# Kernel optimization log

Hardware: AMD Instinct MI355X
Metric: run time of the kernel (lower is better)

## Reference

```python
import jax, jax.numpy as jnp
import numpy as np

N = 100000  # nodes
E = 600000  # edges
D = 128     # input_dim
H = D // 2  # hidden of MLP head
OUT = 10    # output_dim
EPS = 1e-5
NEG_SLOPE = 0.2


def _p(key, shape, scale):
    return jax.random.normal(key, shape, dtype=jnp.float32) * scale


def setup_inputs() -> dict:
    key = jax.random.key(0)
    ks = jax.random.split(key, 16)
    s = 1.0 / np.sqrt(D)
    return {
        "x": jax.random.normal(ks[0], (N, D), dtype=jnp.float32),
        "edge_index": jax.random.randint(ks[1], (2, E), 0, N, dtype=jnp.int64),
        # SAGEConv: lin_l (applied to mean-aggregated neighbors, has bias), lin_r (root)
        "sage_Wl": _p(ks[2], (D, D), s), "sage_Wr": _p(ks[3], (D, D), s),
        "sage_b": jnp.zeros((D,), jnp.float32),
        # GCNConv
        "gcn_W": _p(ks[4], (D, D), s), "gcn_b": jnp.zeros((D,), jnp.float32),
        # GATConv (heads=1)
        "gat_W": _p(ks[5], (D, D), s),
        "gat_att_src": _p(ks[6], (D,), s), "gat_att_dst": _p(ks[7], (D,), s),
        "gat_b": jnp.zeros((D,), jnp.float32),
        # BatchNorms (batch-stat normalization)
        "bn1_g": jnp.ones((D,), jnp.float32), "bn1_b": jnp.zeros((D,), jnp.float32),
        "bn2_g": jnp.ones((D,), jnp.float32), "bn2_b": jnp.zeros((D,), jnp.float32),
        "bn3_g": jnp.ones((D,), jnp.float32), "bn3_b": jnp.zeros((D,), jnp.float32),
        # MLP head
        "lin1_W": _p(ks[8], (D, H), s), "lin1_b": jnp.zeros((H,), jnp.float32),
        "lin2_W": _p(ks[9], (H, OUT), 1.0 / np.sqrt(H)), "lin2_b": jnp.zeros((OUT,), jnp.float32),
    }


def _bn_relu(x, g, b):
    mu = jnp.mean(x, axis=0)
    var = jnp.mean(jnp.square(x - mu), axis=0)
    return jax.nn.relu((x - mu) * jax.lax.rsqrt(var + EPS) * g + b)


def _sage(x, src, dst, Wl, Wr, b):
    agg = jax.ops.segment_sum(x[src], dst, num_segments=N)          # [N, D]
    cnt = jax.ops.segment_sum(jnp.ones((src.shape[0],), x.dtype), dst, num_segments=N)
    mean = agg / jnp.maximum(cnt, 1.0)[:, None]
    return mean @ Wl + x @ Wr + b


def _gcn(x, src, dst, W, b):
    loop = jnp.arange(N, dtype=src.dtype)
    s = jnp.concatenate([src, loop]); d = jnp.concatenate([dst, loop])
    deg = jax.ops.segment_sum(jnp.ones((d.shape[0],), x.dtype), d, num_segments=N)
    dinv = jnp.where(deg > 0, jax.lax.rsqrt(jnp.maximum(deg, 1.0)), 0.0)
    xw = x @ W
    msg = xw[s] * (dinv[s] * dinv[d])[:, None]
    return jax.ops.segment_sum(msg, d, num_segments=N) + b


def _gat(x, src, dst, W, att_s, att_d, b):
    loop = jnp.arange(N, dtype=src.dtype)
    s = jnp.concatenate([src, loop]); d = jnp.concatenate([dst, loop])
    xw = x @ W                                  # [N, D]
    a_s = xw @ att_s                            # [N]
    a_d = xw @ att_d                            # [N]
    e = jax.nn.leaky_relu(a_s[s] + a_d[d], NEG_SLOPE)  # [E+N]
    m = jax.ops.segment_max(e, d, num_segments=N)
    ee = jnp.exp(e - m[d])
    z = jax.ops.segment_sum(ee, d, num_segments=N)
    alpha = ee / z[d]
    return jax.ops.segment_sum(alpha[:, None] * xw[s], d, num_segments=N) + b


def reference(x, edge_index, sage_Wl, sage_Wr, sage_b, gcn_W, gcn_b,
              gat_W, gat_att_src, gat_att_dst, gat_b,
              bn1_g, bn1_b, bn2_g, bn2_b, bn3_g, bn3_b,
              lin1_W, lin1_b, lin2_W, lin2_b):
    src, dst = edge_index[0], edge_index[1]
    h = _bn_relu(_sage(x, src, dst, sage_Wl, sage_Wr, sage_b), bn1_g, bn1_b)
    h = _bn_relu(_gcn(h, src, dst, gcn_W, gcn_b), bn2_g, bn2_b)
    h = _bn_relu(_gat(h, src, dst, gat_W, gat_att_src, gat_att_dst, gat_b), bn3_g, bn3_b)
    # dropout is identity in eval mode
    h = jax.nn.relu(h @ lin1_W + lin1_b) @ lin2_W + lin2_b
    return jax.nn.log_softmax(h, axis=1)
```

## Files before the change

### kernel.cpp

```cpp
#include <hip/hip_runtime.h>

static constexpr int Dd = 128;
static constexpr int Hh = 64;
static constexpr int OC = 10;
#define CDIV(a,b) (((a)+(b)-1)/(b))

typedef __attribute__((ext_vector_type(8))) short short8v;
typedef __attribute__((ext_vector_type(16))) float f32x16;
typedef unsigned short u16;

__device__ __forceinline__ float lrelu(float x){ return x>0.f? x : 0.2f*x; }
__device__ __forceinline__ unsigned f2bf(float f){
  unsigned u = __float_as_uint(f);
  return (u + 0x7FFFu + ((u>>16)&1u)) >> 16;
}
__device__ __forceinline__ float bl(unsigned u){ return __uint_as_float(u<<16); }
__device__ __forceinline__ float bh(unsigned u){ return __uint_as_float(u & 0xFFFF0000u); }

__global__ __launch_bounds__(256) void k_hist(const int* __restrict__ dst, int E,
    int* __restrict__ cnt) {
  int e = blockIdx.x*256 + threadIdx.x;
  if (e < E) atomicAdd(cnt + dst[e], 1);
}

__global__ __launch_bounds__(256) void k_scan_l1(const int* __restrict__ cnt,
    int* __restrict__ rp, int n, int* __restrict__ bsum) {
  __shared__ int sdata[256];
  int t = threadIdx.x;
  int base = blockIdx.x*2048 + t*8;
  int v[8]; int s = 0;
  #pragma unroll
  for (int k = 0; k < 8; k++) { v[k] = (base+k < n) ? cnt[base+k] : 0; s += v[k]; }
  sdata[t] = s; __syncthreads();
  for (int off = 1; off < 256; off <<= 1) {
    int a = sdata[t];
    int b = (t >= off) ? sdata[t-off] : 0;
    __syncthreads();
    sdata[t] = a + b;
    __syncthreads();
  }
  int ex = sdata[t] - s;
  if (t == 255) bsum[blockIdx.x] = sdata[255];
  int run = ex;
  #pragma unroll
  for (int k = 0; k < 8; k++) { if (base+k < n) rp[base+k] = run; run += v[k]; }
}

__global__ void k_scan_l2(int* __restrict__ bsum, int nb) {
  if (threadIdx.x == 0 && blockIdx.x == 0) {
    int run = 0;
    for (int i = 0; i < nb; i++) { int v = bsum[i]; bsum[i] = run; run += v; }
  }
}

__global__ __launch_bounds__(256) void k_scan_l3(int* __restrict__ rp, int n,
    const int* __restrict__ bsum, int E) {
  int off = bsum[blockIdx.x];
  int base = blockIdx.x*2048 + threadIdx.x*8;
  #pragma unroll
  for (int k = 0; k < 8; k++) if (base+k < n) rp[base+k] += off;
  if (blockIdx.x == 0 && threadIdx.x == 0) rp[n] = E;
}

__global__ __launch_bounds__(256) void k_fill(const int* __restrict__ src,
    const int* __restrict__ dst, int E, const int* __restrict__ rp,
    int* __restrict__ cnt, int* __restrict__ col) {
  int e = blockIdx.x*256 + threadIdx.x;
  if (e >= E) return;
  int d = dst[e];
  int pos = rp[d] + atomicSub(cnt + d, 1) - 1;
  col[pos] = src[e];
}

__global__ __launch_bounds__(256) void k_dinv(const int* __restrict__ rp,
    float* __restrict__ dinv, int n) {
  int i = blockIdx.x*256 + threadIdx.x;
  if (i < n) dinv[i] = rsqrtf((float)(rp[i+1] - rp[i]) + 1.0f);
}

__global__ __launch_bounds__(256) void k_wt_all(
    const float* __restrict__ w0, const float* __restrict__ w1,
    const float* __restrict__ w2, const float* __restrict__ w3,
    const float* __restrict__ w4,
    u16* __restrict__ o0, u16* __restrict__ o1, u16* __restrict__ o2,
    u16* __restrict__ o3, u16* __restrict__ o4) {
  int idx = blockIdx.x*256 + threadIdx.x;
  const float* W; u16* O; int base, N;
  if (idx < 65536) {
    int m = idx >> 14;
    W = m==0?w0 : m==1?w1 : m==2?w2 : w3;
    O = m==0?o0 : m==1?o1 : m==2?o2 : o3;
    base = idx & 16383; N = 128;
  } else if (idx < 73728) {
    W = w4; O = o4; base = idx - 65536; N = 64;
  } else return;
  int n = base / 128, k = base % 128;
  int kc = k >> 3, nf = n >> 5, lm = n & 31;
  int fi = (((kc*(N>>5) + nf)*32 + lm) << 3) | (k & 7);
  O[fi] = (u16)f2bf(W[k*N + n]);
}

__global__ __launch_bounds__(256) void k_tobf16(const float* __restrict__ in,
    u16* __restrict__ out, int n8) {
  int idx = blockIdx.x*256 + threadIdx.x;
  if (idx >= n8) return;
  const float4* p = reinterpret_cast<const float4*>(in) + idx*2;
  float4 v0 = p[0], v1 = p[1];
  uint4 w;
  w.x = f2bf(v0.x) | (f2bf(v0.y)<<16);
  w.y = f2bf(v0.z) | (f2bf(v0.w)<<16);
  w.z = f2bf(v1.x) | (f2bf(v1.y)<<16);
  w.w = f2bf(v1.z) | (f2bf(v1.w)<<16);
  reinterpret_cast<uint4*>(out)[idx] = w;
}

__global__ __launch_bounds__(256) void k_sage_gather(const u16* __restrict__ xb,
    const int* __restrict__ rp, const int* __restrict__ col,
    u16* __restrict__ ob, int n) {
  int gid = blockIdx.x*256 + threadIdx.x;
  int i = gid >> 5, l = gid & 31;
  if (i >= n) return;
  int beg = rp[i], end = rp[i+1];
  const u16* xp = xb + l*4;
  float a0=0.f, a1=0.f, a2=0.f, a3=0.f;
  int j = beg;
  if (j + 4 <= end) {
    int s0=col[j], s1=col[j+1], s2=col[j+2], s3=col[j+3];
    uint2 c0 = *reinterpret_cast<const uint2*>(xp + (size_t)s0*Dd);
    uint2 c1 = *reinterpret_cast<const uint2*>(xp + (size_t)s1*Dd);
    uint2 c2 = *reinterpret_cast<const uint2*>(xp + (size_t)s2*Dd);
    uint2 c3 = *reinterpret_cast<const uint2*>(xp + (size_t)s3*Dd);
    j += 4;
    for (; j + 4 <= end; j += 4) {
      int t0=col[j], t1=col[j+1], t2=col[j+2], t3=col[j+3];
      uint2 n0 = *reinterpret_cast<const uint2*>(xp + (size_t)t0*Dd);
      uint2 n1 = *reinterpret_cast<const uint2*>(xp + (size_t)t1*Dd);
      uint2 n2 = *reinterpret_cast<const uint2*>(xp + (size_t)t2*Dd);
      uint2 n3 = *reinterpret_cast<const uint2*>(xp + (size_t)t3*Dd);
      a0 += (bl(c0.x)+bl(c1.x)) + (bl(c2.x)+bl(c3.x));
      a1 += (bh(c0.x)+bh(c1.x)) + (bh(c2.x)+bh(c3.x));
      a2 += (bl(c0.y)+bl(c1.y)) + (bl(c2.y)+bl(c3.y));
      a3 += (bh(c0.y)+bh(c1.y)) + (bh(c2.y)+bh(c3.y));
      c0=n0; c1=n1; c2=n2; c3=n3;
    }
    a0 += (bl(c0.x)+bl(c1.x)) + (bl(c2.x)+bl(c3.x));
    a1 += (bh(c0.x)+bh(c1.x)) + (bh(c2.x)+bh(c3.x));
    a2 += (bl(c0.y)+bl(c1.y)) + (bl(c2.y)+bl(c3.y));
    a3 += (bh(c0.y)+bh(c1.y)) + (bh(c2.y)+bh(c3.y));
  }
  for (; j < end; j++) {
    int s = col[j];
    uint2 v = *reinterpret_cast<const uint2*>(xp + (size_t)s*Dd);
    a0 += bl(v.x); a1 += bh(v.x); a2 += bl(v.y); a3 += bh(v.y);
  }
  float inv = 1.0f / fmaxf((float)(end - beg), 1.0f);
  uint2 o;
  o.x = f2bf(a0*inv) | (f2bf(a1*inv)<<16);
  o.y = f2bf(a2*inv) | (f2bf(a3*inv)<<16);
  *reinterpret_cast<uint2*>(ob + (size_t)i*Dd + l*4) = o;
}

__global__ __launch_bounds__(256) void k_gcn_gather(const u16* __restrict__ xb,
    const int* __restrict__ rp, const int* __restrict__ col,
    const float* __restrict__ dinv, u16* __restrict__ ob, int n) {
  int gid = blockIdx.x*256 + threadIdx.x;
  int i = gid >> 5, l = gid & 31;
  if (i >= n) return;
  int beg = rp[i], end = rp[i+1];
  const u16* xp = xb + l*4;
  float a0=0.f, a1=0.f, a2=0.f, a3=0.f;
  int j = beg;
  if (j + 4 <= end) {
    int s0=col[j], s1=col[j+1], s2=col[j+2], s3=col[j+3];
    uint2 c0 = *reinterpret_cast<const uint2*>(xp + (size_t)s0*Dd);
    uint2 c1 = *reinterpret_cast<const uint2*>(xp + (size_t)s1*Dd);
    uint2 c2 = *reinterpret_cast<const uint2*>(xp + (size_t)s2*Dd);
    uint2 c3 = *reinterpret_cast<const uint2*>(xp + (size_t)s3*Dd);
    float w0 = dinv[s0], w1 = dinv[s1], w2 = dinv[s2], w3 = dinv[s3];
    j += 4;
    for (; j + 4 <= end; j += 4) {
      int t0=col[j], t1=col[j+1], t2=col[j+2], t3=col[j+3];
      uint2 n0 = *reinterpret_cast<const uint2*>(xp + (size_t)t0*Dd);
      uint2 n1 = *reinterpret_cast<const uint2*>(xp + (size_t)t1*Dd);
      uint2 n2 = *reinterpret_cast<const uint2*>(xp + (size_t)t2*Dd);
      uint2 n3 = *reinterpret_cast<const uint2*>(xp + (size_t)t3*Dd);
      float x0 = dinv[t0], x1 = dinv[t1], x2 = dinv[t2], x3 = dinv[t3];
      a0 += (w0*bl(c0.x)+w1*bl(c1.x)) + (w2*bl(c2.x)+w3*bl(c3.x));
      a1 += (w0*bh(c0.x)+w1*bh(c1.x)) + (w2*bh(c2.x)+w3*bh(c3.x));
      a2 += (w0*bl(c0.y)+w1*bl(c1.y)) + (w2*bl(c2.y)+w3*bl(c3.y));
      a3 += (w0*bh(c0.y)+w1*bh(c1.y)) + (w2*bh(c2.y)+w3*bh(c3.y));
      c0=n0; c1=n1; c2=n2; c3=n3;
      w0=x0; w1=x1; w2=x2; w3=x3;
    }
    a0 += (w0*bl(c0.x)+w1*bl(c1.x)) + (w2*bl(c2.x)+w3*bl(c3.x));
    a1 += (w0*bh(c0.x)+w1*bh(c1.x)) + (w2*bh(c2.x)+w3*bh(c3.x));
    a2 += (w0*bl(c0.y)+w1*bl(c1.y)) + (w2*bl(c2.y)+w3*bl(c3.y));
    a3 += (w0*bh(c0.y)+w1*bh(c1.y)) + (w2*bh(c2.y)+w3*bh(c3.y));
  }
  for (; j < end; j++) {
    int s = col[j];
    float w = dinv[s];
    uint2 v = *reinterpret_cast<const uint2*>(xp + (size_t)s*Dd);
    a0 += w*bl(v.x); a1 += w*bh(v.x); a2 += w*bl(v.y); a3 += w*bh(v.y);
  }
  float di = dinv[i];
  float ws = di*di;
  uint2 sv = *reinterpret_cast<const uint2*>(xp + (size_t)i*Dd);
  a0 = di*a0 + ws*bl(sv.x); a1 = di*a1 + ws*bh(sv.x);
  a2 = di*a2 + ws*bl(sv.y); a3 = di*a3 + ws*bh(sv.y);
  uint2 o;
  o.x = f2bf(a0) | (f2bf(a1)<<16);
  o.y = f2bf(a2) | (f2bf(a3)<<16);
  *reinterpret_cast<uint2*>(ob + (size_t)i*Dd + l*4) = o;
}

__global__ __launch_bounds__(256) void k_gat_gather(const u16* __restrict__ xb,
    const int* __restrict__ rp, const int* __restrict__ col,
    const float* __restrict__ a_s, const float* __restrict__ a_d,
    u16* __restrict__ ob, int n) {
  int gid = blockIdx.x*256 + threadIdx.x;
  int i = gid >> 5, l = gid & 31;
  if (i >= n) return;
  int beg = rp[i], end = rp[i+1];
  const u16* xp = xb + l*4;
  float ad = a_d[i];
  float m = lrelu(a_s[i] + ad);
  float z = 1.0f;
  uint2 sv = *reinterpret_cast<const uint2*>(xp + (size_t)i*Dd);
  float a0 = bl(sv.x), a1 = bh(sv.x), a2 = bl(sv.y), a3 = bh(sv.y);
  int j = beg;
  if (j + 4 <= end) {
    int s0=col[j], s1=col[j+1], s2=col[j+2], s3=col[j+3];
    uint2 c0 = *reinterpret_cast<const uint2*>(xp + (size_t)s0*Dd);
    uint2 c1 = *reinterpret_cast<const uint2*>(xp + (size_t)s1*Dd);
    uint2 c2 = *reinterpret_cast<const uint2*>(xp + (size_t)s2*Dd);
    uint2 c3 = *reinterpret_cast<const uint2*>(xp + (size_t)s3*Dd);
    float f0 = a_s[s0], f1 = a_s[s1], f2 = a_s[s2], f3 = a_s[s3];
    j += 4;
    for (; j + 4 <= end; j += 4) {
      int t0=col[j], t1=col[j+1], t2=col[j+2], t3=col[j+3];
      uint2 n0 = *reinterpret_cast<const uint2*>(xp + (size_t)t0*Dd);
      uint2 n1 = *reinterpret_cast<const uint2*>(xp + (size_t)t1*Dd);
      uint2 n2 = *reinterpret_cast<const uint2*>(xp + (size_t)t2*Dd);
      uint2 n3 = *reinterpret_cast<const uint2*>(xp + (size_t)t3*Dd);
      float g0 = a_s[t0], g1 = a_s[t1], g2 = a_s[t2], g3 = a_s[t3];
      float e0 = lrelu(f0+ad), e1 = lrelu(f1+ad);
      float e2 = lrelu(f2+ad), e3 = lrelu(f3+ad);
      float mg = fmaxf(fmaxf(e0,e1), fmaxf(e2,e3));
      if (mg > m) {
        float r = __expf(m - mg);
        z *= r; a0 *= r; a1 *= r; a2 *= r; a3 *= r;
        m = mg;
      }
      float w0 = __expf(e0-m), w1 = __expf(e1-m);
      float w2 = __expf(e2-m), w3 = __expf(e3-m);
      z += (w0+w1) + (w2+w3);
      a0 += (w0*bl(c0.x)+w1*bl(c1.x)) + (w2*bl(c2.x)+w3*bl(c3.x));
      a1 += (w0*bh(c0.x)+w1*bh(c1.x)) + (w2*bh(c2.x)+w3*bh(c3.x));
      a2 += (w0*bl(c0.y)+w1*bl(c1.y)) + (w2*bl(c2.y)+w3*bl(c3.y));
      a3 += (w0*bh(c0.y)+w1*bh(c1.y)) + (w2*bh(c2.y)+w3*bh(c3.y));
      c0=n0; c1=n1; c2=n2; c3=n3;
      f0=g0; f1=g1; f2=g2; f3=g3;
    }
    float e0 = lrelu(f0+ad), e1 = lrelu(f1+ad);
    float e2 = lrelu(f2+ad), e3 = lrelu(f3+ad);
    float mg = fmaxf(fmaxf(e0,e1), fmaxf(e2,e3));
    if (mg > m) {
      float r = __expf(m - mg);
      z *= r; a0 *= r; a1 *= r; a2 *= r; a3 *= r;
      m = mg;
    }
    float w0 = __expf(e0-m), w1 = __expf(e1-m);
    float w2 = __expf(e2-m), w3 = __expf(e3-m);
    z += (w0+w1) + (w2+w3);
    a0 += (w0*bl(c0.x)+w1*bl(c1.x)) + (w2*bl(c2.x)+w3*bl(c3.x));
    a1 += (w0*bh(c0.x)+w1*bh(c1.x)) + (w2*bh(c2.x)+w3*bh(c3.x));
    a2 += (w0*bl(c0.y)+w1*bl(c1.y)) + (w2*bl(c2.y)+w3*bl(c3.y));
    a3 += (w0*bh(c0.y)+w1*bh(c1.y)) + (w2*bh(c2.y)+w3*bh(c3.y));
  }
  for (; j < end; j++) {
    int s = col[j];
    uint2 v = *reinterpret_cast<const uint2*>(xp + (size_t)s*Dd);
    float e = lrelu(a_s[s]+ad);
    if (e > m) {
      float r = __expf(m - e);
      z *= r; a0 *= r; a1 *= r; a2 *= r; a3 *= r;
      m = e;
    }
    float w = __expf(e-m);
    z += w;
    a0 += w*bl(v.x); a1 += w*bh(v.x); a2 += w*bl(v.y); a3 += w*bh(v.y);
  }
  float inv = 1.0f / z;
  uint2 o;
  o.x = f2bf(a0*inv) | (f2bf(a1*inv)<<16);
  o.y = f2bf(a2*inv) | (f2bf(a3*inv)<<16);
  *reinterpret_cast<uint2*>(ob + (size_t)i*Dd + l*4) = o;
}

__global__ __launch_bounds__(256) void k_bn_stats_bf(const u16* __restrict__ X, int M,
    float* __restrict__ gsum, float* __restrict__ gsq) {
  __shared__ float ss[2][256];
  int t = threadIdx.x;
  int cd = t & 63;
  int rg = t >> 6;
  float s0=0.f, q0=0.f, s1=0.f, q1=0.f;
  const unsigned* Xu = reinterpret_cast<const unsigned*>(X);
  for (int r = blockIdx.x*4 + rg; r < M; r += gridDim.x*4) {
    unsigned v = Xu[(size_t)r*64 + cd];
    float a = bl(v), b = bh(v);
    s0 += a; q0 += a*a; s1 += b; q1 += b*b;
  }
  ss[0][t] = s0; ss[1][t] = q0; __syncthreads();
  float rs0 = 0.f, rq0 = 0.f;
  if (rg == 0) {
    rs0 = ss[0][cd] + ss[0][cd+64] + ss[0][cd+128] + ss[0][cd+192];
    rq0 = ss[1][cd] + ss[1][cd+64] + ss[1][cd+128] + ss[1][cd+192];
  }
  __syncthreads();
  ss[0][t] = s1; ss[1][t] = q1; __syncthreads();
  if (rg == 0) {
    float rs1 = ss[0][cd] + ss[0][cd+64] + ss[0][cd+128] + ss[0][cd+192];
    float rq1 = ss[1][cd] + ss[1][cd+64] + ss[1][cd+128] + ss[1][cd+192];
    atomicAdd(gsum + 2*cd,     rs0); atomicAdd(gsq + 2*cd,     rq0);
    atomicAdd(gsum + 2*cd + 1, rs1); atomicAdd(gsq + 2*cd + 1, rq1);
  }
}

template<int NCOLS, bool DUAL, bool BNA, bool STATS, bool BIASRELU, bool ATT, bool OUTBF, bool HEAD>
__global__ __launch_bounds__(256) void k_mm(
    const u16* __restrict__ A1, const u16* __restrict__ A2,
    const u16* __restrict__ WT1, const u16* __restrict__ WT2,
    const float* __restrict__ bng, const float* __restrict__ bnb,
    const float* __restrict__ bsum_in, const float* __restrict__ bsq_in,
    const float* __restrict__ bias,
    void* __restrict__ Cout, int M,
    float* __restrict__ gsum, float* __restrict__ gsq,
    const float* __restrict__ att_sv, const float* __restrict__ att_dv,
    float* __restrict__ as_out, float* __restrict__ ad_out,
    const float* __restrict__ W2, const float* __restrict__ b2) {
  constexpr int NF = NCOLS/32;
  __shared__ char ldsA[128*272];
  __shared__ char ldsW[NCOLS*256];
  __shared__ float s_scale[128], s_shift[128];
  __shared__ float s_sum[128], s_sq[128];
  __shared__ float w2s[Hh][OC];
  __shared__ float b2s[OC];
  int t = threadIdx.x;
  int wave = t >> 6, l = t & 63;
  int lm = l & 31, h = l >> 5;
  int row0 = blockIdx.x*128;

  if constexpr (BNA) {
    if (t < 128) {
      float mu = bsum_in[t] / (float)M;
      float var = fmaxf(bsq_in[t] / (float)M - mu*mu, 0.f);
      float sc = bng[t] * rsqrtf(var + 1e-5f);
      s_scale[t] = sc;
      s_shift[t] = bnb[t] - mu*sc;
    }
  }
  if constexpr (STATS) {
    if (t < 128) { s_sum[t] = 0.f; s_sq[t] = 0.f; }
  }
  if constexpr (HEAD) {
    for (int i = t; i < Hh*OC; i += 256) w2s[i/OC][i%OC] = W2[i];
    if (t < OC) b2s[t] = b2[t];
  }
  if (BNA || STATS || HEAD) __syncthreads();

  f32x16 acc[NF];
  #pragma unroll
  for (int nf = 0; nf < NF; nf++)
    #pragma unroll
    for (int i = 0; i < 16; i++) acc[nf][i] = 0.f;

  const int nph = DUAL ? 2 : 1;
  for (int ph = 0; ph < nph; ph++) {
    if (ph) __syncthreads();
    const u16* A = (DUAL && ph) ? A2 : A1;
    const u16* WT = (DUAL && ph) ? WT2 : WT1;
    #pragma unroll
    for (int i = 0; i < 8; i++) {
      int c = i*256 + t; int row = c >> 4; int k0 = (c & 15) << 3;
      uint4 w = {0,0,0,0};
      if (row0 + row < M)
        w = *reinterpret_cast<const uint4*>(A + (size_t)(row0+row)*128 + k0);
      if constexpr (BNA) {
        float4 sc0 = *reinterpret_cast<const float4*>(&s_scale[k0]);
        float4 sc1 = *reinterpret_cast<const float4*>(&s_scale[k0+4]);
        float4 sh0 = *reinterpret_cast<const float4*>(&s_shift[k0]);
        float4 sh1 = *reinterpret_cast<const float4*>(&s_shift[k0+4]);
        float e0 = fmaxf(bl(w.x)*sc0.x+sh0.x, 0.f), e1 = fmaxf(bh(w.x)*sc0.y+sh0.y, 0.f);
        float e2 = fmaxf(bl(w.y)*sc0.z+sh0.z, 0.f), e3 = fmaxf(bh(w.y)*sc0.w+sh0.w, 0.f);
        float e4 = fmaxf(bl(w.z)*sc1.x+sh1.x, 0.f), e5 = fmaxf(bh(w.z)*sc1.y+sh1.y, 0.f);
        float e6 = fmaxf(bl(w.w)*sc1.z+sh1.z, 0.f), e7 = fmaxf(bh(w.w)*sc1.w+sh1.w, 0.f);
        w.x = f2bf(e0) | (f2bf(e1)<<16);
        w.y = f2bf(e2) | (f2bf(e3)<<16);
        w.z = f2bf(e4) | (f2bf(e5)<<16);
        w.w = f2bf(e6) | (f2bf(e7)<<16);
      }
      *reinterpret_cast<uint4*>(ldsA + row*272 + k0*2) = w;
    }
    #pragma unroll
    for (int i = 0; i < NCOLS/16; i++) {
      int c = i*256 + t;
      reinterpret_cast<uint4*>(ldsW)[c] = reinterpret_cast<const uint4*>(WT)[c];
    }
    __syncthreads();
    #pragma unroll
    for (int ks = 0; ks < 8; ks++) {
      int kc = ks*2 + h;
      int arow = wave*32 + lm;
      short8v af = *reinterpret_cast<short8v*>(ldsA + arow*272 + kc*16);
      #pragma unroll
      for (int nf = 0; nf < NF; nf++) {
        short8v bf = *reinterpret_cast<short8v*>(ldsW + ((kc*NF + nf)*32 + lm)*16);
        acc[nf] = __builtin_amdgcn_mfma_f32_32x32x16_bf16(af, bf, acc[nf], 0, 0, 0);
      }
    }
  }
  if constexpr (HEAD) {
    __syncthreads();
    float* mrow = reinterpret_cast<float*>(ldsA);
    #pragma unroll
    for (int nf = 0; nf < NF; nf++) {
      int colg = nf*32 + lm;
      float bv = bias[colg];
      #pragma unroll
      for (int reg = 0; reg < 16; reg++) {
        int row = wave*32 + (reg&3) + 8*(reg>>2) + 4*h;
        mrow[row*65 + colg] = fmaxf(acc[nf][reg] + bv, 0.f);
      }
    }
    __syncthreads();
    if (t < 128) {
      int row = row0 + t;
      if (row < M) {
        float p[OC];
        #pragma unroll
        for (int c = 0; c < OC; c++) p[c] = b2s[c];
        for (int k = 0; k < Hh; k++) {
          float a = mrow[t*65 + k];
          #pragma unroll
          for (int c = 0; c < OC; c++) p[c] += a * w2s[k][c];
        }
        float mx = p[0];
        #pragma unroll
        for (int c = 1; c < OC; c++) mx = fmaxf(mx, p[c]);
        float s = 0.f;
        #pragma unroll
        for (int c = 0; c < OC; c++) s += __expf(p[c] - mx);
        float lse = mx + __logf(s);
        #pragma unroll
        for (int c = 0; c < OC; c++)
          ((float*)Cout)[(size_t)row*OC + c] = p[c] - lse;
      }
    }
    return;
  }
  #pragma unroll
  for (int nf = 0; nf < NF; nf++) {
    int colg = nf*32 + lm;
    float bv = 0.f;
    if constexpr (BIASRELU) bv = bias[colg];
    float ps = 0.f, pq = 0.f;
    #pragma unroll
    for (int reg = 0; reg < 16; reg++) {
      int row = row0 + wave*32 + (reg&3) + 8*(reg>>2) + 4*h;
      float v = acc[nf][reg];
      if constexpr (BIASRELU) v = fmaxf(v + bv, 0.f);
      if (row < M) {
        if constexpr (OUTBF)
          ((u16*)Cout)[(size_t)row*NCOLS + colg] = (u16)f2bf(v);
        else
          ((float*)Cout)[(size_t)row*NCOLS + colg] = v;
      }
      ps += v; pq += v*v;
    }
    if constexpr (STATS) {
      atomicAdd(&s_sum[colg], ps);
      atomicAdd(&s_sq[colg], pq);
    }
  }
  if constexpr (ATT) {
    float as_c[NF], ad_c[NF];
    #pragma unroll
    for (int nf = 0; nf < NF; nf++) { as_c[nf] = att_sv[nf*32+lm]; ad_c[nf] = att_dv[nf*32+lm]; }
    #pragma unroll
    for (int reg = 0; reg < 16; reg++) {
      float ps = 0.f, pd = 0.f;
      #pragma unroll
      for (int nf = 0; nf < NF; nf++) { float v = acc[nf][reg]; ps += v*as_c[nf]; pd += v*ad_c[nf]; }
      #pragma unroll
      for (int mm = 1; mm < 32; mm <<= 1) { ps += __shfl_xor(ps, mm); pd += __shfl_xor(pd, mm); }
      int row = row0 + wave*32 + (reg&3) + 8*(reg>>2) + 4*h;
      if (lm == 0 && row < M) { as_out[row] = ps; ad_out[row] = pd; }
    }
  }
  if constexpr (STATS) {
    __syncthreads();
    if (t < 128) { atomicAdd(gsum + t, s_sum[t]); atomicAdd(gsq + t, s_sq[t]); }
  }
}

extern "C" void kernel_launch(void* const* d_in, const int* in_sizes, int n_in,
                              void* d_out, int out_size, void* d_ws, size_t ws_size,
                              hipStream_t stream) {
  const float* x       = (const float*)d_in[0];
  const int*   ei      = (const int*)d_in[1];
  const float* sage_Wl = (const float*)d_in[2];
  const float* sage_Wr = (const float*)d_in[3];
  const float* gcn_W   = (const float*)d_in[5];
  const float* gat_W   = (const float*)d_in[7];
  const float* att_s   = (const float*)d_in[8];
  const float* att_d   = (const float*)d_in[9];
  const float* bn1_g = (const float*)d_in[11], *bn1_b = (const float*)d_in[12];
  const float* bn2_g = (const float*)d_in[13], *bn2_b = (const float*)d_in[14];
  const float* bn3_g = (const float*)d_in[15], *bn3_b = (const float*)d_in[16];
  const float* lin1_W = (const float*)d_in[17], *lin1_b = (const float*)d_in[18];
  const float* lin2_W = (const float*)d_in[19], *lin2_b = (const float*)d_in[20];

  const int Nn = in_sizes[0] / Dd;
  const int Ee = in_sizes[1] / 2;
  const int* srcv = ei;
  const int* dstv = ei + Ee;

  u16* b0 = (u16*)d_ws;
  u16* b1 = b0 + (size_t)Nn*Dd;
  u16* b2 = b1 + (size_t)Nn*Dd;
  float* dinv  = (float*)(b2 + (size_t)Nn*Dd);
  float* a_s   = dinv + Nn;
  float* a_d   = a_s + Nn;
  float* bs    = a_d + Nn;
  float* bs1_sum = bs,        *bs1_sq = bs + 128;
  float* bs2_sum = bs + 256,  *bs2_sq = bs + 384;
  float* bs3_sum = bs + 512,  *bs3_sq = bs + 640;
  int* rp    = (int*)(bs + 768);
  int* cnt_i = rp + (Nn + 1);
  int* bsum  = cnt_i + Nn;
  int* col   = bsum + 64;
  u16* wt_sWl = (u16*)(col + Ee);
  u16* wt_sWr = wt_sWl + 128*128;
  u16* wt_gcn = wt_sWr + 128*128;
  u16* wt_gat = wt_gcn + 128*128;
  u16* wt_l1  = wt_gat + 128*128;

  const dim3 B(256);
  const dim3 Gn(CDIV(Nn, 256));
  const dim3 Gn32(CDIV(Nn*32, 256));
  const dim3 Ge(CDIV(Ee, 256));
  const dim3 Gmm(CDIV(Nn, 128));
  const dim3 Gstat(512);
  const int nscan = CDIV(Nn, 2048);

  hipMemsetAsync(cnt_i, 0, (size_t)Nn*sizeof(int), stream);
  hipMemsetAsync(bs, 0, 768*sizeof(float), stream);

  k_hist<<<Ge, B, 0, stream>>>(dstv, Ee, cnt_i);
  k_scan_l1<<<dim3(nscan), B, 0, stream>>>(cnt_i, rp, Nn, bsum);
  k_scan_l2<<<dim3(1), dim3(64), 0, stream>>>(bsum, nscan);
  k_scan_l3<<<dim3(nscan), B, 0, stream>>>(rp, Nn, bsum, Ee);
  k_fill<<<Ge, B, 0, stream>>>(srcv, dstv, Ee, rp, cnt_i, col);
  k_dinv<<<Gn, B, 0, stream>>>(rp, dinv, Nn);
  k_wt_all<<<dim3(288), B, 0, stream>>>(sage_Wl, sage_Wr, gcn_W, gat_W, lin1_W,
                                        wt_sWl, wt_sWr, wt_gcn, wt_gat, wt_l1);
  k_tobf16<<<dim3(CDIV(Nn*Dd/8, 256)), B, 0, stream>>>(x, b0, Nn*Dd/8);

  k_sage_gather<<<Gn32, B, 0, stream>>>(b0, rp, col, b1, Nn);
  k_mm<128, true, false, true, false, false, true, false><<<Gmm, B, 0, stream>>>(
      b1, b0, wt_sWl, wt_sWr, nullptr, nullptr, nullptr, nullptr, nullptr,
      b2, Nn, bs1_sum, bs1_sq, nullptr, nullptr, nullptr, nullptr, nullptr, nullptr);

  k_mm<128, false, true, false, false, false, true, false><<<Gmm, B, 0, stream>>>(
      b2, nullptr, wt_gcn, nullptr, bn1_g, bn1_b, bs1_sum, bs1_sq, nullptr,
      b0, Nn, nullptr, nullptr, nullptr, nullptr, nullptr, nullptr, nullptr, nullptr);
  k_gcn_gather<<<Gn32, B, 0, stream>>>(b0, rp, col, dinv, b1, Nn);
  k_bn_stats_bf<<<Gstat, B, 0, stream>>>(b1, Nn, bs2_sum, bs2_sq);

  k_mm<128, false, true, false, false, true, true, false><<<Gmm, B, 0, stream>>>(
      b1, nullptr, wt_gat, nullptr, bn2_g, bn2_b, bs2_sum, bs2_sq, nullptr,
      b2, Nn, nullptr, nullptr, att_s, att_d, a_s, a_d, nullptr, nullptr);
  k_gat_gather<<<Gn32, B, 0, stream>>>(b2, rp, col, a_s, a_d, b0, Nn);
  k_bn_stats_bf<<<Gstat, B, 0, stream>>>(b0, Nn, bs3_sum, bs3_sq);

  k_mm<64, false, true, false, true, false, false, true><<<Gmm, B, 0, stream>>>(
      b0, nullptr, wt_l1, nullptr, bn3_g, bn3_b, bs3_sum, bs3_sq, lin1_b,
      (float*)d_out, Nn, nullptr, nullptr, nullptr, nullptr, nullptr, nullptr,
      lin2_W, lin2_b);
}
```

Measured before the change: 379.8 us.

## Stream GEMM weights through LDS in halves and merge shared scratch arrays

Weights are re-laid out nf-major so each GEMM block can load half the output columns' weights into LDS at a time, halving the ldsW footprint. The separate BN scale/shift, stats and head-weight shared arrays are merged into one aux buffer to cut LDS further. The aim is higher occupancy (more blocks per CU) in the fused GEMM kernels. The cost is an extra barrier and a second weight load per phase.

```diff
diff --git a/kernel.cpp b/kernel.cpp
--- a/kernel.cpp
+++ b/kernel.cpp
@@ -96,7 +96,7 @@
   } else return;
   int n = base / 128, k = base % 128;
   int kc = k >> 3, nf = n >> 5, lm = n & 31;
-  int fi = (((kc*(N>>5) + nf)*32 + lm) << 3) | (k & 7);
+  int fi = (((nf*16 + kc)*32 + lm) << 3) | (k & 7);
   O[fi] = (u16)f2bf(W[k*N + n]);
 }
 
@@ -339,13 +339,11 @@
     const float* __restrict__ att_sv, const float* __restrict__ att_dv,
     float* __restrict__ as_out, float* __restrict__ ad_out,
     const float* __restrict__ W2, const float* __restrict__ b2) {
-  constexpr int NF = NCOLS/32;
+  constexpr int NF  = NCOLS/32;
+  constexpr int NFH = NF/2;
   __shared__ char ldsA[128*272];
-  __shared__ char ldsW[NCOLS*256];
-  __shared__ float s_scale[128], s_shift[128];
-  __shared__ float s_sum[128], s_sq[128];
-  __shared__ float w2s[Hh][OC];
-  __shared__ float b2s[OC];
+  __shared__ char ldsW[NFH*16*32*16];
+  __shared__ float s_aux[640];
   int t = threadIdx.x;
   int wave = t >> 6, l = t & 63;
   int lm = l & 31, h = l >> 5;
@@ -356,18 +354,14 @@
       float mu = bsum_in[t] / (float)M;
       float var = fmaxf(bsq_in[t] / (float)M - mu*mu, 0.f);
       float sc = bng[t] * rsqrtf(var + 1e-5f);
-      s_scale[t] = sc;
-      s_shift[t] = bnb[t] - mu*sc;
+      s_aux[t] = sc;
+      s_aux[128 + t] = bnb[t] - mu*sc;
     }
   }
   if constexpr (STATS) {
-    if (t < 128) { s_sum[t] = 0.f; s_sq[t] = 0.f; }
-  }
-  if constexpr (HEAD) {
-    for (int i = t; i < Hh*OC; i += 256) w2s[i/OC][i%OC] = W2[i];
-    if (t < OC) b2s[t] = b2[t];
-  }
-  if (BNA || STATS || HEAD) __syncthreads();
+    if (t < 128) { s_aux[256 + t] = 0.f; s_aux[384 + t] = 0.f; }
+  }
+  if (BNA || STATS) __syncthreads();
 
   f32x16 acc[NF];
   #pragma unroll
@@ -387,10 +381,10 @@
       if (row0 + row < M)
         w = *reinterpret_cast<const uint4*>(A + (size_t)(row0+row)*128 + k0);
       if constexpr (BNA) {
-        float4 sc0 = *reinterpret_cast<const float4*>(&s_scale[k0]);
-        float4 sc1 = *reinterpret_cast<const float4*>(&s_scale[k0+4]);
-        float4 sh0 = *reinterpret_cast<const float4*>(&s_shift[k0]);
-        float4 sh1 = *reinterpret_cast<const float4*>(&s_shift[k0+4]);
+        float4 sc0 = *reinterpret_cast<const float4*>(&s_aux[k0]);
+        float4 sc1 = *reinterpret_cast<const float4*>(&s_aux[k0+4]);
+        float4 sh0 = *reinterpret_cast<const float4*>(&s_aux[128+k0]);
+        float4 sh1 = *reinterpret_cast<const float4*>(&s_aux[128+k0+4]);
         float e0 = fmaxf(bl(w.x)*sc0.x+sh0.x, 0.f), e1 = fmaxf(bh(w.x)*sc0.y+sh0.y, 0.f);
         float e2 = fmaxf(bl(w.y)*sc0.z+sh0.z, 0.f), e3 = fmaxf(bh(w.y)*sc0.w+sh0.w, 0.f);
         float e4 = fmaxf(bl(w.z)*sc1.x+sh1.x, 0.f), e5 = fmaxf(bh(w.z)*sc1.y+sh1.y, 0.f);
@@ -403,20 +397,25 @@
       *reinterpret_cast<uint4*>(ldsA + row*272 + k0*2) = w;
     }
     #pragma unroll
-    for (int i = 0; i < NCOLS/16; i++) {
-      int c = i*256 + t;
-      reinterpret_cast<uint4*>(ldsW)[c] = reinterpret_cast<const uint4*>(WT)[c];
-    }
-    __syncthreads();
-    #pragma unroll
-    for (int ks = 0; ks < 8; ks++) {
-      int kc = ks*2 + h;
-      int arow = wave*32 + lm;
-      short8v af = *reinterpret_cast<short8v*>(ldsA + arow*272 + kc*16);
+    for (int wh = 0; wh < 2; wh++) {
+      if (wh) __syncthreads();
+      const uint4* wsrc = reinterpret_cast<const uint4*>(WT + (size_t)wh*NFH*4096);
       #pragma unroll
-      for (int nf = 0; nf < NF; nf++) {
-        short8v bf = *reinterpret_cast<short8v*>(ldsW + ((kc*NF + nf)*32 + lm)*16);
-        acc[nf] = __builtin_amdgcn_mfma_f32_32x32x16_bf16(af, bf, acc[nf], 0, 0, 0);
+      for (int i = 0; i < NFH*4; i++) {
+        int c = i*256 + t;
+        reinterpret_cast<uint4*>(ldsW)[c] = wsrc[c];
+      }
+      __syncthreads();
+      #pragma unroll
+      for (int ks = 0; ks < 8; ks++) {
+        int kc = ks*2 + h;
+        int arow = wave*32 + lm;
+        short8v af = *reinterpret_cast<short8v*>(ldsA + arow*272 + kc*16);
+        #pragma unroll
+        for (int nfh = 0; nfh < NFH; nfh++) {
+          short8v bf = *reinterpret_cast<short8v*>(ldsW + ((nfh*16 + kc)*32 + lm)*16);
+          acc[wh*NFH + nfh] = __builtin_amdgcn_mfma_f32_32x32x16_bf16(af, bf, acc[wh*NFH + nfh], 0, 0, 0);
+        }
       }
     }
   }
@@ -433,17 +432,18 @@
         mrow[row*65 + colg] = fmaxf(acc[nf][reg] + bv, 0.f);
       }
     }
+    for (int i = t; i < Hh*OC; i += 256) s_aux[i] = W2[i];
     __syncthreads();
     if (t < 128) {
       int row = row0 + t;
       if (row < M) {
         float p[OC];
         #pragma unroll
-        for (int c = 0; c < OC; c++) p[c] = b2s[c];
+        for (int c = 0; c < OC; c++) p[c] = b2[c];
         for (int k = 0; k < Hh; k++) {
           float a = mrow[t*65 + k];
           #pragma unroll
-          for (int c = 0; c < OC; c++) p[c] += a * w2s[k][c];
+          for (int c = 0; c < OC; c++) p[c] += a * s_aux[k*OC + c];
         }
         float mx = p[0];
         #pragma unroll
@@ -479,8 +479,8 @@
       ps += v; pq += v*v;
     }
     if constexpr (STATS) {
-      atomicAdd(&s_sum[colg], ps);
-      atomicAdd(&s_sq[colg], pq);
+      atomicAdd(&s_aux[256 + colg], ps);
+      atomicAdd(&s_aux[384 + colg], pq);
     }
   }
   if constexpr (ATT) {
@@ -500,7 +500,7 @@
   }
   if constexpr (STATS) {
     __syncthreads();
-    if (t < 128) { atomicAdd(gsum + t, s_sum[t]); atomicAdd(gsq + t, s_sq[t]); }
+    if (t < 128) { atomicAdd(gsum + t, s_aux[256 + t]); atomicAdd(gsq + t, s_aux[384 + t]); }
   }
 }
 
```

Result: slower. 390.6 us (+2.9%).
